# Kernel optimization log

Measured on AMD Instinct MI355X. Metric: run time of the kernel, lower is better.

Reference implementation:

```python
import jax, jax.numpy as jnp
import numpy as np

B, H, W, DIM = 32, 56, 56, 192
WSZ = 7
HEADS = 8
DK = 32
DV = 32
INNER_K = HEADS * DK  # 256
INNER_V = HEADS * DV  # 256


def setup_inputs() -> dict:
    key = jax.random.key(0)
    ks = jax.random.split(key, 8)
    s = 0.05
    return {
        "x": jax.random.normal(ks[0], (B, H, W, DIM), jnp.float32),
        "Wq": jax.random.normal(ks[1], (DIM, INNER_K), jnp.float32) * s,
        "Wk": jax.random.normal(ks[2], (DIM, INNER_K), jnp.float32) * s,
        "Wv": jax.random.normal(ks[3], (DIM, INNER_V), jnp.float32) * s,
        "Wlocal": jax.random.normal(ks[4], (3, 3, INNER_V, INNER_V), jnp.float32) * s,
        "b_local": jnp.zeros((INNER_V,), jnp.float32),
        "Wout": jax.random.normal(ks[5], (INNER_V, DIM), jnp.float32) * s,
        "b_out": jnp.zeros((DIM,), jnp.float32),
    }


def _window(t, heads, wsz):
    # (b, H, W, heads*d) -> (b*nx*ny, heads, wsz*wsz, d)
    b, h, w, c = t.shape
    d = c // heads
    nx, ny = h // wsz, w // wsz
    t = t.reshape(b, nx, wsz, ny, wsz, heads, d)
    t = t.transpose(0, 1, 3, 5, 2, 4, 6)
    return t.reshape(b * nx * ny, heads, wsz * wsz, d)


def reference(x, Wq, Wk, Wv, Wlocal, b_local, Wout, b_out):
    scale = DK ** (-0.5)
    # 1x1 convs == per-pixel matmuls
    q = jnp.einsum('bhwc,cd->bhwd', x, Wq)
    k = jnp.einsum('bhwc,cd->bhwd', x, Wk)
    v = jnp.einsum('bhwc,cd->bhwd', x, Wv)
    # 3x3 local interactive conv on v (SAME padding)
    local_out = jax.lax.conv_general_dilated(
        v, Wlocal, window_strides=(1, 1), padding='SAME',
        dimension_numbers=('NHWC', 'HWIO', 'NHWC')) + b_local
    # window partition
    qw = _window(q, HEADS, WSZ)
    kw = _window(k, HEADS, WSZ)
    vw = _window(v, HEADS, WSZ)
    dots = jnp.einsum('bhid,bhjd->bhij', qw, kw) * scale  # (B*nx*ny, heads, 49, 49)
    attn = jax.nn.softmax(dots, axis=-1)
    out = jnp.einsum('bhij,bhjd->bhid', attn, vw)
    # window merge: (b*nx*ny, heads, wsz*wsz, d) -> (b, H, W, heads*d)
    nx, ny = H // WSZ, W // WSZ
    out = out.reshape(B, nx, ny, HEADS, WSZ, WSZ, DV)
    out = out.transpose(0, 1, 4, 2, 5, 3, 6).reshape(B, H, W, HEADS * DV)
    out = out + local_out
    out = jnp.einsum('bhwc,cd->bhwd', out, Wout) + b_out
    return out
```

## Files before the change

### kernel.cpp

```cpp
#include <hip/hip_runtime.h>

typedef unsigned short ushort_t;
typedef __bf16  bf16x8 __attribute__((ext_vector_type(8)));
typedef float   f32x4  __attribute__((ext_vector_type(4)));
typedef unsigned short u16x8 __attribute__((ext_vector_type(8)));

#define MFMA16(a,b,c) __builtin_amdgcn_mfma_f32_16x16x32_bf16((a),(b),(c),0,0,0)
#define WAITVM(N) asm volatile("s_waitcnt vmcnt(" #N ")" ::: "memory")
#define BARRIER() do{ __builtin_amdgcn_s_barrier(); asm volatile("" ::: "memory"); }while(0)

static __device__ __forceinline__ ushort_t f2bf(float f){
  __bf16 h = (__bf16)f;
  return __builtin_bit_cast(ushort_t, h);
}
static __device__ __forceinline__ float bf2f(ushort_t b){
  union{unsigned u; float f;} x; x.u = ((unsigned)b)<<16; return x.f;
}
static __device__ __forceinline__ bf16x8 ldg_bf8(const ushort_t* p, bool valid){
  u16x8 r = {0,0,0,0,0,0,0,0};
  if(valid) r = *(const u16x8*)p;
  return __builtin_bit_cast(bf16x8, r);
}
static __device__ __forceinline__ bf16x8 ldg_bf8u(const ushort_t* p){
  u16x8 r = *(const u16x8*)p;
  return __builtin_bit_cast(bf16x8, r);
}
static __device__ __forceinline__ bf16x8 lds_bf8(const ushort_t* p){
  u16x8 r = *(const u16x8*)p;
  return __builtin_bit_cast(bf16x8, r);
}
static __device__ __forceinline__ void gload_lds16(const ushort_t* g, ushort_t* l){
  __builtin_amdgcn_global_load_lds(
      (const __attribute__((address_space(1))) void*)g,
      (__attribute__((address_space(3))) void*)l, 16, 0, 0);
}

__global__ __launch_bounds__(256) void prep_kernel(
    const float* __restrict__ x,
    const float* __restrict__ Wq, const float* __restrict__ Wk,
    const float* __restrict__ Wv, const float* __restrict__ Wl,
    const float* __restrict__ Wo,
    ushort_t* __restrict__ qkvT, ushort_t* __restrict__ wlT,
    ushort_t* __restrict__ woT, ushort_t* __restrict__ xbf)
{
  int idx = blockIdx.x*256 + threadIdx.x;
  if(idx < 147456){
    int n = idx/192, kk = idx%192;
    const float* W = (n < 256) ? Wq : ((n < 512) ? Wk : Wv);
    qkvT[idx] = f2bf(W[kk*256 + (n & 255)]);
  } else if(idx < 147456 + 589824){
    int t2 = idx - 147456;
    int j   = t2 & 7;
    int sl  = (t2 >> 3) & 3;
    int col = (t2 >> 5) & 255;
    int ks  = (t2 >> 13) & 7;
    int tap = t2 >> 16;
    int grp = sl ^ ((col>>1)&3);
    int k = ks*32 + grp*8 + j;
    wlT[t2] = f2bf(Wl[((size_t)tap*256 + k)*256 + col]);
  } else if(idx < 737280 + 49152){
    int t3 = idx - 737280;
    int col = t3/256, kk = t3%256;
    woT[t3] = f2bf(Wo[kk*192 + col]);
  } else {
    int c = idx - 786432;
    int row = c/24, cp = c%24;
    int sc = cp ^ (row&7);
    const float* src = x + (size_t)row*192 + sc*8;
    float4 f0 = *(const float4*)src;
    float4 f1 = *(const float4*)(src+4);
    u16x8 o;
    o[0]=f2bf(f0.x); o[1]=f2bf(f0.y); o[2]=f2bf(f0.z); o[3]=f2bf(f0.w);
    o[4]=f2bf(f1.x); o[5]=f2bf(f1.y); o[6]=f2bf(f1.z); o[7]=f2bf(f1.w);
    *(u16x8*)&xbf[(size_t)c*8] = o;
  }
}

__global__ __launch_bounds__(256,4) void qkv_kernel(
    const ushort_t* __restrict__ xbf, const ushort_t* __restrict__ WT,
    ushort_t* __restrict__ q, ushort_t* __restrict__ kbuf,
    ushort_t* __restrict__ vbuf)
{
  __shared__ ushort_t aLds[64*192];
  const int m0 = blockIdx.x * 64;
  const int which = blockIdx.y;
  ushort_t* O = (which==0) ? q : ((which==1) ? kbuf : vbuf);
  const int tid = threadIdx.x;
  const int l = tid & 63, w = tid >> 6;
  const int lr = l&15, g = l>>4;
  #pragma unroll
  for(int r=0;r<6;++r){
    gload_lds16(xbf + (size_t)m0*192 + (size_t)(tid + r*256)*8,
                aLds + (size_t)(r*256 + w*64)*8);
  }
  __syncthreads();

  const ushort_t* Wbase = WT + (size_t)(which*256 + w*64)*192;
  f32x4 acc[4][4];
  #pragma unroll
  for(int mi=0;mi<4;++mi)
    #pragma unroll
    for(int nj=0;nj<4;++nj){ f32x4 z={0.f,0.f,0.f,0.f}; acc[mi][nj]=z; }

  bf16x8 bA[4], bB[4];
  #pragma unroll
  for(int nj=0;nj<4;++nj) bA[nj] = ldg_bf8u(Wbase + (size_t)(nj*16+lr)*192 + g*8);

  #pragma unroll
  for(int ks2=0; ks2<3; ++ks2){
    int ks0 = 2*ks2, ks1 = 2*ks2+1;
    #pragma unroll
    for(int nj=0;nj<4;++nj) bB[nj] = ldg_bf8u(Wbase + (size_t)(nj*16+lr)*192 + ks1*32 + g*8);
    #pragma unroll
    for(int mi=0;mi<4;++mi){
      int row = mi*16 + lr;
      bf16x8 af = lds_bf8(&aLds[(row*192 + ks0*32 + g*8) ^ ((row&7)<<3)]);
      #pragma unroll
      for(int nj=0;nj<4;++nj) acc[mi][nj] = MFMA16(af, bA[nj], acc[mi][nj]);
    }
    if(ks2<2){
      #pragma unroll
      for(int nj=0;nj<4;++nj) bA[nj] = ldg_bf8u(Wbase + (size_t)(nj*16+lr)*192 + (ks1+1)*32 + g*8);
    }
    #pragma unroll
    for(int mi=0;mi<4;++mi){
      int row = mi*16 + lr;
      bf16x8 af = lds_bf8(&aLds[(row*192 + ks1*32 + g*8) ^ ((row&7)<<3)]);
      #pragma unroll
      for(int nj=0;nj<4;++nj) acc[mi][nj] = MFMA16(af, bB[nj], acc[mi][nj]);
    }
  }
  #pragma unroll
  for(int mi=0;mi<4;++mi)
    #pragma unroll
    for(int nj=0;nj<4;++nj){
      int col = w*64 + nj*16 + lr;
      #pragma unroll
      for(int i=0;i<4;++i){
        int row = mi*16 + g*4 + i;
        O[(size_t)(m0+row)*256 + col] = f2bf(acc[mi][nj][i]);
      }
    }
}

__global__ __launch_bounds__(256,2) void conv_kernel(
    const ushort_t* __restrict__ v, const ushort_t* __restrict__ WlT,
    const float* __restrict__ b_local, ushort_t* __restrict__ local_out)
{
  __shared__ ushort_t aBuf[2][256*32];
  __shared__ ushort_t bBuf[3][256*32];
  const int bid = blockIdx.x;
  const int tile = (bid & 7) * 98 + (bid >> 3);
  const int p0 = tile * 128;
  const int tid = threadIdx.x;
  const int l = tid&63, w=tid>>6, wm=w>>1, wn=w&1, lr=l&15, g=l>>4;

  unsigned maskbits[4];
  int pxloc[4];
  #pragma unroll
  for(int mi=0;mi<4;++mi){
    int p = p0 + wm*64 + mi*16 + lr;
    int rem = p % 3136;
    int y = rem/56, x = rem%56;
    unsigned mb = 0;
    #pragma unroll
    for(int tap=0;tap<9;++tap){
      int dy = tap/3 - 1, dx = tap%3 - 1;
      if(((unsigned)(y+dy) < 56u) && ((unsigned)(x+dx) < 56u)) mb |= (1u<<tap);
    }
    maskbits[mi] = mb;
    pxloc[mi] = wm*64 + mi*16 + lr + 64;
  }

  auto stageA = [&](int ks, ushort_t* dst){
    #pragma unroll
    for(int r=0;r<4;++r){
      int c = tid + r*256;
      int px = c>>2, sl = c&3;
      int px_abs = p0 - 64 + px;
      px_abs = min(max(px_abs, 0), 100351);
      int chunk = sl ^ ((px>>1)&3);
      gload_lds16(v + (size_t)px_abs*256 + ks*32 + chunk*8,
                  dst + (size_t)(r*256 + w*64)*8);
    }
  };
  auto stageB = [&](int ks, int tap, ushort_t* dst){
    const ushort_t* src = WlT + ((size_t)tap*8 + ks)*8192;
    #pragma unroll
    for(int r=0;r<4;++r){
      gload_lds16(src + (size_t)(tid + r*256)*8,
                  dst + (size_t)(r*256 + w*64)*8);
    }
  };

  f32x4 acc[4][8];
  #pragma unroll
  for(int mi=0;mi<4;++mi)
    #pragma unroll
    for(int nj=0;nj<8;++nj){ f32x4 z={0.f,0.f,0.f,0.f}; acc[mi][nj]=z; }

  auto compute = [&](int tap, const ushort_t* aL, const ushort_t* bL){
    int shift = (tap/3 - 1)*56 + (tap%3 - 1);
    bf16x8 af[4];
    #pragma unroll
    for(int mi=0;mi<4;++mi){
      int px = pxloc[mi] + shift;
      int sl = g ^ ((px>>1)&3);
      u16x8 rv = *(const u16x8*)&aL[px*32 + sl*8];
      if(!((maskbits[mi]>>tap)&1)){ u16x8 z={0,0,0,0,0,0,0,0}; rv=z; }
      af[mi] = __builtin_bit_cast(bf16x8, rv);
    }
    __builtin_amdgcn_s_setprio(1);
    #pragma unroll
    for(int nj=0;nj<8;++nj){
      int col = wn*128 + nj*16 + lr;
      int slb = g ^ ((col>>1)&3);
      bf16x8 bfr = lds_bf8(&bL[col*32 + slb*8]);
      #pragma unroll
      for(int mi=0;mi<4;++mi) acc[mi][nj] = MFMA16(af[mi], bfr, acc[mi][nj]);
    }
    __builtin_amdgcn_s_setprio(0);
  };

  stageA(0, aBuf[0]);
  stageB(0, 0, bBuf[0]);
  stageB(0, 1, bBuf[1]);

  for(int ks=0; ks<7; ++ks){
    #pragma unroll
    for(int tap=0; tap<9; ++tap){
      if(tap==1) WAITVM(8); else WAITVM(4);
      BARRIER();
      if(tap==0) stageA(ks+1, aBuf[(ks+1)&1]);
      stageB(ks + (tap+2)/9, (tap+2)%9, bBuf[(tap+2)%3]);
      compute(tap, aBuf[ks&1], bBuf[tap%3]);
    }
  }
  #pragma unroll
  for(int tap=0; tap<9; ++tap){
    if(tap==8) WAITVM(0); else WAITVM(4);
    BARRIER();
    if(tap<7) stageB(7, tap+2, bBuf[(tap+2)%3]);
    compute(tap, aBuf[1], bBuf[tap%3]);
  }

  #pragma unroll
  for(int nj=0;nj<8;++nj){
    int col = wn*128 + nj*16 + lr;
    float bb = b_local[col];
    #pragma unroll
    for(int mi=0;mi<4;++mi)
      #pragma unroll
      for(int i=0;i<4;++i){
        int p = p0 + wm*64 + mi*16 + g*4 + i;
        local_out[(size_t)p*256 + col] = f2bf(acc[mi][nj][i] + bb);
      }
  }
}

__global__ __launch_bounds__(256) void attn_kernel(
    const ushort_t* __restrict__ q, const ushort_t* __restrict__ k,
    const ushort_t* __restrict__ v, ushort_t* __restrict__ out)
{
  __shared__ ushort_t pLds[4*64*64];
  __shared__ ushort_t vLds[4*32*64];
  const int tid = threadIdx.x;
  const int w = tid>>6, l = tid&63, lr = l&15, g = l>>4;
  const int gid = blockIdx.x*4 + w;
  const int win = gid>>3, head = gid&7;
  const int b = win>>6, rem = win&63, wy = rem>>3, wx = rem&7;
  const size_t base = (size_t)b*3136 + wy*7*56 + wx*7;
  ushort_t* pl = pLds + w*4096;
  ushort_t* vl = vLds + w*2048;
  {
    int p = l;
    bool valid = p < 49;
    const ushort_t* vp = v + (base + (p/7)*56 + (p%7))*256 + head*32;
    #pragma unroll
    for(int d0=0; d0<32; d0+=8){
      u16x8 rv = {0,0,0,0,0,0,0,0};
      if(valid) rv = *(const u16x8*)(vp + d0);
      #pragma unroll
      for(int j=0;j<8;++j){
        int d = d0+j;
        vl[(d*64 + p) ^ ((d&7)<<3)] = valid ? rv[j] : (ushort_t)0;
      }
    }
  }
  f32x4 dot[4][4];
  #pragma unroll
  for(int mi=0;mi<4;++mi)
    #pragma unroll
    for(int nj=0;nj<4;++nj){ f32x4 z={0.f,0.f,0.f,0.f}; dot[mi][nj]=z; }
  bf16x8 qf[4], kf[4];
  #pragma unroll
  for(int t=0;t<4;++t){
    int p = t*16 + lr; bool valid = p<49;
    size_t pix = base + (p/7)*56 + (p%7);
    qf[t] = ldg_bf8(q + pix*256 + head*32 + g*8, valid);
    kf[t] = ldg_bf8(k + pix*256 + head*32 + g*8, valid);
  }
  #pragma unroll
  for(int mi=0;mi<4;++mi)
    #pragma unroll
    for(int nj=0;nj<4;++nj)
      dot[mi][nj] = MFMA16(qf[mi], kf[nj], dot[mi][nj]);
  const float sc = 0.17677669529663687f * 1.4426950408889634f;
  float rs[4][4];
  #pragma unroll
  for(int mi=0;mi<4;++mi){
    #pragma unroll
    for(int i=0;i<4;++i){
      float m = -1e30f;
      #pragma unroll
      for(int nj=0;nj<4;++nj){
        int col = nj*16 + lr;
        if(col < 49) m = fmaxf(m, dot[mi][nj][i]);
      }
      m = fmaxf(m, __shfl_xor(m,1));
      m = fmaxf(m, __shfl_xor(m,2));
      m = fmaxf(m, __shfl_xor(m,4));
      m = fmaxf(m, __shfl_xor(m,8));
      float e[4]; float s = 0.f;
      #pragma unroll
      for(int nj=0;nj<4;++nj){
        int col = nj*16 + lr;
        e[nj] = (col < 49) ? exp2f((dot[mi][nj][i]-m)*sc) : 0.f;
        s += e[nj];
      }
      s += __shfl_xor(s,1); s += __shfl_xor(s,2);
      s += __shfl_xor(s,4); s += __shfl_xor(s,8);
      rs[mi][i] = s;
      int row = mi*16 + g*4 + i;
      #pragma unroll
      for(int nj=0;nj<4;++nj){
        int col = nj*16 + lr;
        pl[(row*64 + col) ^ ((row&7)<<3)] = f2bf(e[nj]);
      }
    }
  }
  __syncthreads();
  f32x4 o[4][2];
  #pragma unroll
  for(int mi=0;mi<4;++mi)
    #pragma unroll
    for(int nj=0;nj<2;++nj){ f32x4 z={0.f,0.f,0.f,0.f}; o[mi][nj]=z; }
  #pragma unroll
  for(int ks=0;ks<2;++ks){
    bf16x8 pa[4];
    #pragma unroll
    for(int mi=0;mi<4;++mi){
      int row = mi*16 + lr;
      pa[mi] = lds_bf8(&pl[(row*64 + ks*32 + g*8) ^ ((row&7)<<3)]);
    }
    #pragma unroll
    for(int nj=0;nj<2;++nj){
      int d = nj*16 + lr;
      bf16x8 vb = lds_bf8(&vl[(d*64 + ks*32 + g*8) ^ ((d&7)<<3)]);
      #pragma unroll
      for(int mi=0;mi<4;++mi) o[mi][nj] = MFMA16(pa[mi], vb, o[mi][nj]);
    }
  }
  #pragma unroll
  for(int mi=0;mi<4;++mi){
    #pragma unroll
    for(int i=0;i<4;++i){
      int row = mi*16 + g*4 + i;
      if(row < 49){
        size_t pix = base + (row/7)*56 + (row%7);
        float inv = 1.0f / rs[mi][i];
        #pragma unroll
        for(int nj=0;nj<2;++nj){
          out[pix*256 + head*32 + nj*16 + lr] = f2bf(o[mi][nj][i] * inv);
        }
      }
    }
  }
}

__global__ __launch_bounds__(256) void outproj_kernel(
    const ushort_t* __restrict__ attn, const ushort_t* __restrict__ local,
    const ushort_t* __restrict__ WoT, const float* __restrict__ b_out,
    float* __restrict__ out)
{
  __shared__ ushort_t aLds[128*256];
  const int m0 = blockIdx.x*128;
  const int tid = threadIdx.x;
  #pragma unroll
  for(int it=0; it<16; ++it){
    int c = tid + it*256;
    int row = c >> 5, cc = c & 31;
    size_t off = (size_t)(m0+row)*256 + cc*8;
    u16x8 a = *(const u16x8*)(attn + off);
    u16x8 bl = *(const u16x8*)(local + off);
    u16x8 o;
    #pragma unroll
    for(int j=0;j<8;++j) o[j] = f2bf(bf2f(a[j]) + bf2f(bl[j]));
    *(u16x8*)&aLds[(row*256 + cc*8) ^ ((row&7)<<3)] = o;
  }
  __syncthreads();
  const int l = tid&63, w = tid>>6, wm=w>>1, wn=w&1, lr=l&15, g=l>>4;
  f32x4 acc[4][6];
  #pragma unroll
  for(int mi=0;mi<4;++mi)
    #pragma unroll
    for(int nj=0;nj<6;++nj){ f32x4 z={0.f,0.f,0.f,0.f}; acc[mi][nj]=z; }
  #pragma unroll
  for(int ks=0;ks<8;++ks){
    bf16x8 af[4];
    #pragma unroll
    for(int mi=0;mi<4;++mi){
      int row = wm*64 + mi*16 + lr;
      af[mi] = lds_bf8(&aLds[(row*256 + ks*32 + g*8) ^ ((row&7)<<3)]);
    }
    #pragma unroll
    for(int nj=0;nj<6;++nj){
      int col = wn*96 + nj*16 + lr;
      bf16x8 bfr = ldg_bf8u(WoT + (size_t)col*256 + ks*32 + g*8);
      #pragma unroll
      for(int mi=0;mi<4;++mi) acc[mi][nj] = MFMA16(af[mi], bfr, acc[mi][nj]);
    }
  }
  #pragma unroll
  for(int nj=0;nj<6;++nj){
    int col = wn*96 + nj*16 + lr;
    float bb = b_out[col];
    #pragma unroll
    for(int mi=0;mi<4;++mi)
      #pragma unroll
      for(int i=0;i<4;++i){
        int row = wm*64 + mi*16 + g*4 + i;
        out[(size_t)(m0+row)*192 + col] = acc[mi][nj][i] + bb;
      }
  }
}

extern "C" void kernel_launch(void* const* d_in, const int* in_sizes, int n_in,
                              void* d_out, int out_size, void* d_ws, size_t ws_size,
                              hipStream_t stream)
{
  const float* x  = (const float*)d_in[0];
  const float* Wq = (const float*)d_in[1];
  const float* Wk = (const float*)d_in[2];
  const float* Wv = (const float*)d_in[3];
  const float* Wl = (const float*)d_in[4];
  const float* bl = (const float*)d_in[5];
  const float* Wo = (const float*)d_in[6];
  const float* bo = (const float*)d_in[7];
  float* out = (float*)d_out;
  char* ws = (char*)d_ws;
  ushort_t* q    = (ushort_t*)(ws);
  ushort_t* kbuf = (ushort_t*)(ws + 51380224);
  ushort_t* vbuf = (ushort_t*)(ws + 102760448);
  ushort_t* attn = (ushort_t*)(ws + 154140672);
  ushort_t* locl = (ushort_t*)(ws + 205520896);
  ushort_t* qkvT = (ushort_t*)(ws + 256901120);
  ushort_t* wlT  = (ushort_t*)(ws + 257196032);
  ushort_t* woT  = (ushort_t*)(ws + 258375680);
  ushort_t* xbf  = attn;

  prep_kernel<<<12480, 256, 0, stream>>>(x, Wq, Wk, Wv, Wl, Wo, qkvT, wlT, woT, xbf);
  qkv_kernel<<<dim3(1568,3), 256, 0, stream>>>(xbf, qkvT, q, kbuf, vbuf);
  conv_kernel<<<784, 256, 0, stream>>>(vbuf, wlT, bl, locl);
  attn_kernel<<<4096, 256, 0, stream>>>(q, kbuf, vbuf, attn);
  outproj_kernel<<<784, 256, 0, stream>>>(attn, locl, woT, bo, out);
}
```

Measured before the change: 343.6 us.

## Load conv weight fragments directly into registers instead of staging through LDS

The 3x3 conv kernel no longer stages Wlocal tiles into a triple-buffered LDS ring. Each wave now loads its B fragments straight from global memory into registers, double-buffered across taps. The A tile is still staged in LDS, prefetched at tap 7, and synchronised with a single __syncthreads per k-step. This removes LDS traffic and most barriers for B, at the cost of more VGPRs and of global-load latency sitting directly on the MFMA path. Weights are re-read per wave from L2, so there is also a synchronisation concern about the stageA prefetch relative to the barrier.

Measured after the change: 471.9 us. 37.3% more time.

```diff
diff --git a/kernel.cpp b/kernel.cpp
--- a/kernel.cpp
+++ b/kernel.cpp
@@ -6,8 +6,6 @@
 typedef unsigned short u16x8 __attribute__((ext_vector_type(8)));
 
 #define MFMA16(a,b,c) __builtin_amdgcn_mfma_f32_16x16x32_bf16((a),(b),(c),0,0,0)
-#define WAITVM(N) asm volatile("s_waitcnt vmcnt(" #N ")" ::: "memory")
-#define BARRIER() do{ __builtin_amdgcn_s_barrier(); asm volatile("" ::: "memory"); }while(0)
 
 static __device__ __forceinline__ ushort_t f2bf(float f){
   __bf16 h = (__bf16)f;
@@ -148,7 +146,6 @@
     const float* __restrict__ b_local, ushort_t* __restrict__ local_out)
 {
   __shared__ ushort_t aBuf[2][256*32];
-  __shared__ ushort_t bBuf[3][256*32];
   const int bid = blockIdx.x;
   const int tile = (bid & 7) * 98 + (bid >> 3);
   const int p0 = tile * 128;
@@ -170,6 +167,14 @@
     }
     maskbits[mi] = mb;
     pxloc[mi] = wm*64 + mi*16 + lr + 64;
+  }
+
+  unsigned bOff[8];
+  #pragma unroll
+  for(int nj=0;nj<8;++nj){
+    int col = wn*128 + nj*16 + lr;
+    int slb = g ^ ((col>>1)&3);
+    bOff[nj] = col*32 + slb*8;
   }
 
   auto stageA = [&](int ks, ushort_t* dst){
@@ -184,14 +189,6 @@
                   dst + (size_t)(r*256 + w*64)*8);
     }
   };
-  auto stageB = [&](int ks, int tap, ushort_t* dst){
-    const ushort_t* src = WlT + ((size_t)tap*8 + ks)*8192;
-    #pragma unroll
-    for(int r=0;r<4;++r){
-      gload_lds16(src + (size_t)(tid + r*256)*8,
-                  dst + (size_t)(r*256 + w*64)*8);
-    }
-  };
 
   f32x4 acc[4][8];
   #pragma unroll
@@ -199,49 +196,48 @@
     #pragma unroll
     for(int nj=0;nj<8;++nj){ f32x4 z={0.f,0.f,0.f,0.f}; acc[mi][nj]=z; }
 
-  auto compute = [&](int tap, const ushort_t* aL, const ushort_t* bL){
-    int shift = (tap/3 - 1)*56 + (tap%3 - 1);
-    bf16x8 af[4];
-    #pragma unroll
-    for(int mi=0;mi<4;++mi){
-      int px = pxloc[mi] + shift;
-      int sl = g ^ ((px>>1)&3);
-      u16x8 rv = *(const u16x8*)&aL[px*32 + sl*8];
-      if(!((maskbits[mi]>>tap)&1)){ u16x8 z={0,0,0,0,0,0,0,0}; rv=z; }
-      af[mi] = __builtin_bit_cast(bf16x8, rv);
-    }
-    __builtin_amdgcn_s_setprio(1);
-    #pragma unroll
-    for(int nj=0;nj<8;++nj){
-      int col = wn*128 + nj*16 + lr;
-      int slb = g ^ ((col>>1)&3);
-      bf16x8 bfr = lds_bf8(&bL[col*32 + slb*8]);
-      #pragma unroll
-      for(int mi=0;mi<4;++mi) acc[mi][nj] = MFMA16(af[mi], bfr, acc[mi][nj]);
-    }
-    __builtin_amdgcn_s_setprio(0);
-  };
-
+  bf16x8 bCur[8], bNxt[8];
+  #pragma unroll
+  for(int nj=0;nj<8;++nj) bCur[nj] = ldg_bf8u(WlT + bOff[nj]);
+  #pragma unroll
+  for(int nj=0;nj<8;++nj) bNxt[nj] = bCur[nj];
   stageA(0, aBuf[0]);
-  stageB(0, 0, bBuf[0]);
-  stageB(0, 1, bBuf[1]);
-
-  for(int ks=0; ks<7; ++ks){
+
+  for(int ks=0; ks<8; ++ks){
+    __syncthreads();
+    const ushort_t* aL = aBuf[ks&1];
+    const ushort_t* Bks = WlT + (size_t)ks*8192;
     #pragma unroll
     for(int tap=0; tap<9; ++tap){
-      if(tap==1) WAITVM(8); else WAITVM(4);
-      BARRIER();
-      if(tap==0) stageA(ks+1, aBuf[(ks+1)&1]);
-      stageB(ks + (tap+2)/9, (tap+2)%9, bBuf[(tap+2)%3]);
-      compute(tap, aBuf[ks&1], bBuf[tap%3]);
-    }
-  }
-  #pragma unroll
-  for(int tap=0; tap<9; ++tap){
-    if(tap==8) WAITVM(0); else WAITVM(4);
-    BARRIER();
-    if(tap<7) stageB(7, tap+2, bBuf[(tap+2)%3]);
-    compute(tap, aBuf[1], bBuf[tap%3]);
+      if(tap < 8){
+        #pragma unroll
+        for(int nj=0;nj<8;++nj)
+          bNxt[nj] = ldg_bf8u(Bks + (size_t)(tap+1)*65536 + bOff[nj]);
+      } else if(ks < 7){
+        #pragma unroll
+        for(int nj=0;nj<8;++nj)
+          bNxt[nj] = ldg_bf8u(Bks + 8192 + bOff[nj]);
+      }
+      if(tap==7 && ks<7) stageA(ks+1, aBuf[(ks+1)&1]);
+      int shift = (tap/3 - 1)*56 + (tap%3 - 1);
+      bf16x8 af[4];
+      #pragma unroll
+      for(int mi=0;mi<4;++mi){
+        int px = pxloc[mi] + shift;
+        int sl = g ^ ((px>>1)&3);
+        u16x8 rv = *(const u16x8*)&aL[px*32 + sl*8];
+        if(!((maskbits[mi]>>tap)&1)){ u16x8 z={0,0,0,0,0,0,0,0}; rv=z; }
+        af[mi] = __builtin_bit_cast(bf16x8, rv);
+      }
+      __builtin_amdgcn_s_setprio(1);
+      #pragma unroll
+      for(int nj=0;nj<8;++nj)
+        #pragma unroll
+        for(int mi=0;mi<4;++mi) acc[mi][nj] = MFMA16(af[mi], bCur[nj], acc[mi][nj]);
+      __builtin_amdgcn_s_setprio(0);
+      #pragma unroll
+      for(int nj=0;nj<8;++nj) bCur[nj] = bNxt[nj];
+    }
   }
 
   #pragma unroll
```

## Fuse local-conv residual add into attention epilogue and slim out-projection tiles

Applied to the files above, without the earlier changes.

The attention kernel now reads the local conv output, adds it to the normalized attention result, and writes the sum in a pre-swizzled layout. This removes the separate attn+local read-and-add pass from the out-projection kernel. The out-projection now stages that buffer into LDS with direct global-to-LDS loads, uses 64-row tiles with each wave covering 48 columns, doubles the grid, and sets a launch bound of 4 for occupancy. The cost is scattered 2-byte reads of the local buffer inside the attention epilogue.

Result: no change. 336.9 us (-1.9%).

```diff
diff --git a/kernel.cpp b/kernel.cpp
--- a/kernel.cpp
+++ b/kernel.cpp
@@ -260,7 +260,8 @@
 
 __global__ __launch_bounds__(256) void attn_kernel(
     const ushort_t* __restrict__ q, const ushort_t* __restrict__ k,
-    const ushort_t* __restrict__ v, ushort_t* __restrict__ out)
+    const ushort_t* __restrict__ v, const ushort_t* __restrict__ locl,
+    ushort_t* __restrict__ sum)
 {
   __shared__ ushort_t pLds[4*64*64];
   __shared__ ushort_t vLds[4*32*64];
@@ -369,67 +370,67 @@
       if(row < 49){
         size_t pix = base + (row/7)*56 + (row%7);
         float inv = 1.0f / rs[mi][i];
+        int swz = (int)(pix & 7);
         #pragma unroll
         for(int nj=0;nj<2;++nj){
-          out[pix*256 + head*32 + nj*16 + lr] = f2bf(o[mi][nj][i] * inv);
+          int e = head*32 + nj*16 + lr;
+          float val = o[mi][nj][i] * inv + bf2f(locl[pix*256 + e]);
+          int es = (((e>>3) ^ swz)<<3) | (e & 7);
+          sum[pix*256 + es] = f2bf(val);
         }
       }
     }
   }
 }
 
-__global__ __launch_bounds__(256) void outproj_kernel(
-    const ushort_t* __restrict__ attn, const ushort_t* __restrict__ local,
-    const ushort_t* __restrict__ WoT, const float* __restrict__ b_out,
-    float* __restrict__ out)
-{
-  __shared__ ushort_t aLds[128*256];
-  const int m0 = blockIdx.x*128;
+__global__ __launch_bounds__(256,4) void outproj_kernel(
+    const ushort_t* __restrict__ sum, const ushort_t* __restrict__ WoT,
+    const float* __restrict__ b_out, float* __restrict__ out)
+{
+  __shared__ ushort_t aLds[64*256];
+  const int m0 = blockIdx.x * 64;
   const int tid = threadIdx.x;
-  #pragma unroll
-  for(int it=0; it<16; ++it){
-    int c = tid + it*256;
-    int row = c >> 5, cc = c & 31;
-    size_t off = (size_t)(m0+row)*256 + cc*8;
-    u16x8 a = *(const u16x8*)(attn + off);
-    u16x8 bl = *(const u16x8*)(local + off);
-    u16x8 o;
-    #pragma unroll
-    for(int j=0;j<8;++j) o[j] = f2bf(bf2f(a[j]) + bf2f(bl[j]));
-    *(u16x8*)&aLds[(row*256 + cc*8) ^ ((row&7)<<3)] = o;
+  const int l = tid&63, w = tid>>6, lr=l&15, g=l>>4;
+  #pragma unroll
+  for(int r=0;r<8;++r){
+    gload_lds16(sum + (size_t)m0*256 + (size_t)(tid + r*256)*8,
+                aLds + (size_t)(r*256 + w*64)*8);
   }
   __syncthreads();
-  const int l = tid&63, w = tid>>6, wm=w>>1, wn=w&1, lr=l&15, g=l>>4;
-  f32x4 acc[4][6];
-  #pragma unroll
-  for(int mi=0;mi<4;++mi)
-    #pragma unroll
-    for(int nj=0;nj<6;++nj){ f32x4 z={0.f,0.f,0.f,0.f}; acc[mi][nj]=z; }
+
+  const ushort_t* Wbase = WoT + (size_t)(w*48)*256;
+  f32x4 acc[4][3];
+  #pragma unroll
+  for(int mi=0;mi<4;++mi)
+    #pragma unroll
+    for(int nj=0;nj<3;++nj){ f32x4 z={0.f,0.f,0.f,0.f}; acc[mi][nj]=z; }
+
   #pragma unroll
   for(int ks=0;ks<8;++ks){
+    bf16x8 bfr[3];
+    #pragma unroll
+    for(int nj=0;nj<3;++nj)
+      bfr[nj] = ldg_bf8u(Wbase + (size_t)(nj*16+lr)*256 + ks*32 + g*8);
     bf16x8 af[4];
     #pragma unroll
     for(int mi=0;mi<4;++mi){
-      int row = wm*64 + mi*16 + lr;
+      int row = mi*16 + lr;
       af[mi] = lds_bf8(&aLds[(row*256 + ks*32 + g*8) ^ ((row&7)<<3)]);
     }
     #pragma unroll
-    for(int nj=0;nj<6;++nj){
-      int col = wn*96 + nj*16 + lr;
-      bf16x8 bfr = ldg_bf8u(WoT + (size_t)col*256 + ks*32 + g*8);
-      #pragma unroll
-      for(int mi=0;mi<4;++mi) acc[mi][nj] = MFMA16(af[mi], bfr, acc[mi][nj]);
-    }
-  }
-  #pragma unroll
-  for(int nj=0;nj<6;++nj){
-    int col = wn*96 + nj*16 + lr;
+    for(int nj=0;nj<3;++nj)
+      #pragma unroll
+      for(int mi=0;mi<4;++mi) acc[mi][nj] = MFMA16(af[mi], bfr[nj], acc[mi][nj]);
+  }
+  #pragma unroll
+  for(int nj=0;nj<3;++nj){
+    int col = w*48 + nj*16 + lr;
     float bb = b_out[col];
     #pragma unroll
     for(int mi=0;mi<4;++mi)
       #pragma unroll
       for(int i=0;i<4;++i){
-        int row = wm*64 + mi*16 + g*4 + i;
+        int row = mi*16 + g*4 + i;
         out[(size_t)(m0+row)*192 + col] = acc[mi][nj][i] + bb;
       }
   }
@@ -452,16 +453,16 @@
   ushort_t* q    = (ushort_t*)(ws);
   ushort_t* kbuf = (ushort_t*)(ws + 51380224);
   ushort_t* vbuf = (ushort_t*)(ws + 102760448);
-  ushort_t* attn = (ushort_t*)(ws + 154140672);
+  ushort_t* sum  = (ushort_t*)(ws + 154140672);
   ushort_t* locl = (ushort_t*)(ws + 205520896);
   ushort_t* qkvT = (ushort_t*)(ws + 256901120);
   ushort_t* wlT  = (ushort_t*)(ws + 257196032);
   ushort_t* woT  = (ushort_t*)(ws + 258375680);
-  ushort_t* xbf  = attn;
+  ushort_t* xbf  = sum;
 
   prep_kernel<<<12480, 256, 0, stream>>>(x, Wq, Wk, Wv, Wl, Wo, qkvT, wlT, woT, xbf);
   qkv_kernel<<<dim3(1568,3), 256, 0, stream>>>(xbf, qkvT, q, kbuf, vbuf);
   conv_kernel<<<784, 256, 0, stream>>>(vbuf, wlT, bl, locl);
-  attn_kernel<<<4096, 256, 0, stream>>>(q, kbuf, vbuf, attn);
-  outproj_kernel<<<784, 256, 0, stream>>>(attn, locl, woT, bo, out);
-}
+  attn_kernel<<<4096, 256, 0, stream>>>(q, kbuf, vbuf, locl, sum);
+  outproj_kernel<<<1568, 256, 0, stream>>>(sum, woT, bo, out);
+}
```
